# Kernel tuning notes

Measured on AMD Instinct MI355X. Metric: run time of the kernel, lower is better.

Reference implementation:

```python
import jax, jax.numpy as jnp
import numpy as np

B, DZ, M_, N_ = 2048, 256, 64, 64
GAMMA, EPS, MAXITERS = 1.0, 1e-6, 1000


def sinkhorn(Mcost):
    # entropic OT with uniform marginals r=1/m, c=1/n (ddn sinkhorn, non-logspace)
    b, h, w = Mcost.shape
    r = 1.0 / h
    c = 1.0 / w
    P = jnp.exp(-GAMMA * Mcost)
    P = P / jnp.sum(P, axis=(1, 2), keepdims=True)

    def cond_fn(state):
        P, it, err = state
        return jnp.logical_and(it < MAXITERS, err > EPS)

    def body_fn(state):
        P, it, _ = state
        alpha = jnp.sum(P, axis=2, keepdims=True)   # row sums (B,h,1)
        P = P * (r / alpha)                          # row normalize to r
        beta = jnp.sum(P, axis=1, keepdims=True)    # col sums (B,1,w)
        err = jnp.max(jnp.abs(beta - c))
        # torch loop breaks BEFORE col-normalizing when converged
        P = jnp.where(err <= EPS, P, P * (c / beta))
        return P, it + 1, err

    init_err = jnp.array(jnp.inf, dtype=Mcost.dtype)
    P, _, _ = jax.lax.while_loop(cond_fn, body_fn, (P, jnp.array(0, jnp.int32), init_err))
    return P


def setup_inputs() -> dict:
    key = jax.random.key(0)
    ks = jax.random.split(key, 7)
    H = M_ * N_
    z = jax.random.normal(ks[0], (B, DZ), dtype=jnp.float32)
    W1 = jax.random.normal(ks[1], (DZ, H), dtype=jnp.float32) * (1.0 / np.sqrt(DZ))
    b1 = jnp.zeros((H,), jnp.float32)
    W2 = jax.random.normal(ks[2], (H, H), dtype=jnp.float32) * (1.0 / np.sqrt(H))
    b2 = jnp.zeros((H,), jnp.float32)
    W3 = jax.random.normal(ks[3], (H, H), dtype=jnp.float32) * (1.0 / np.sqrt(H))
    b3 = jnp.zeros((H,), jnp.float32)
    return {"z": z, "W1": W1, "b1": b1, "W2": W2, "b2": b2, "W3": W3, "b3": b3}


def reference(z, W1, b1, W2, b2, W3, b3):
    x = jax.nn.relu(z @ W1 + b1)
    x = jax.nn.relu(x @ W2 + b2)
    x = x @ W3 + b3
    x = x.reshape(z.shape[0], M_, N_)  # (B, m, n) cost matrix
    return sinkhorn(x)
```

## Files before the change

kernel.cpp:

```cpp
#include <hip/hip_runtime.h>
#include <hip/hip_bf16.h>

typedef unsigned short ushort_t;
typedef __attribute__((ext_vector_type(8))) short bf16x8;
typedef __attribute__((ext_vector_type(4))) float f32x4;

#define MDIM 2048
#define NDIM 4096

__device__ __forceinline__ ushort_t to_bf16(float f) {
    __hip_bfloat16 h = __float2bfloat16(f);
    return *reinterpret_cast<ushort_t*>(&h);
}

__global__ void cast_bf16_kernel(const float* __restrict__ in, ushort_t* __restrict__ out, int n) {
    int i = blockIdx.x * blockDim.x + threadIdx.x;
    if (i < n) out[i] = to_bf16(in[i]);
}

__global__ void transpose_cast_kernel(const float* __restrict__ W, ushort_t* __restrict__ WT,
                                      int K, int N) {
    __shared__ float tile[32][33];
    const int tx = threadIdx.x, ty = threadIdx.y;
    const int n0 = blockIdx.x * 32, k0 = blockIdx.y * 32;
#pragma unroll
    for (int r = 0; r < 4; ++r)
        tile[ty + r * 8][tx] = W[(size_t)(k0 + ty + r * 8) * N + n0 + tx];
    __syncthreads();
    const int t = ty * 32 + tx;
    const int nl = t >> 3;
    const int kc = (t & 7) * 4;
    ushort4 o;
    o.x = to_bf16(tile[kc + 0][nl]);
    o.y = to_bf16(tile[kc + 1][nl]);
    o.z = to_bf16(tile[kc + 2][nl]);
    o.w = to_bf16(tile[kc + 3][nl]);
    *reinterpret_cast<ushort4*>(&WT[(size_t)(n0 + nl) * K + k0 + kc]) = o;
}

template <typename OutT, bool RELU>
__global__ __launch_bounds__(256, 2) void gemm_bt(const ushort_t* __restrict__ A,
                                                  const ushort_t* __restrict__ BT,
                                                  const float* __restrict__ bias,
                                                  OutT* __restrict__ C, int Kdim) {
    __shared__ __align__(16) ushort_t As[128 * 40];
    __shared__ __align__(16) ushort_t Bs[128 * 40];

    const int t = threadIdx.x;
    const int m0 = blockIdx.y * 128;
    const int n0 = blockIdx.x * 128;
    const int lane = t & 63;
    const int wid = t >> 6;
    const int quad = lane >> 4;
    const int l16 = lane & 15;
    const int wm = (wid & 1) * 64;
    const int wn = (wid >> 1) * 64;

    f32x4 acc[4][4];
#pragma unroll
    for (int i = 0; i < 4; ++i)
#pragma unroll
        for (int j = 0; j < 4; ++j) acc[i][j] = (f32x4){0.f, 0.f, 0.f, 0.f};

    const int row_a = t >> 2;
    const int cc = t & 3;

    const ushort_t* pA0 = A + (size_t)(m0 + row_a) * Kdim + cc * 8;
    const ushort_t* pA1 = A + (size_t)(m0 + row_a + 64) * Kdim + cc * 8;
    const ushort_t* pB0 = BT + (size_t)(n0 + row_a) * Kdim + cc * 8;
    const ushort_t* pB1 = BT + (size_t)(n0 + row_a + 64) * Kdim + cc * 8;

    uint4 av0 = *reinterpret_cast<const uint4*>(pA0);
    uint4 av1 = *reinterpret_cast<const uint4*>(pA1);
    uint4 bv0 = *reinterpret_cast<const uint4*>(pB0);
    uint4 bv1 = *reinterpret_cast<const uint4*>(pB1);

    for (int k0 = 0; k0 < Kdim; k0 += 32) {
        __syncthreads();
        *reinterpret_cast<uint4*>(&As[row_a * 40 + cc * 8]) = av0;
        *reinterpret_cast<uint4*>(&As[(row_a + 64) * 40 + cc * 8]) = av1;
        *reinterpret_cast<uint4*>(&Bs[row_a * 40 + cc * 8]) = bv0;
        *reinterpret_cast<uint4*>(&Bs[(row_a + 64) * 40 + cc * 8]) = bv1;
        __syncthreads();

        if (k0 + 32 < Kdim) {
            av0 = *reinterpret_cast<const uint4*>(pA0 + k0 + 32);
            av1 = *reinterpret_cast<const uint4*>(pA1 + k0 + 32);
            bv0 = *reinterpret_cast<const uint4*>(pB0 + k0 + 32);
            bv1 = *reinterpret_cast<const uint4*>(pB1 + k0 + 32);
        }

        bf16x8 af[4], bfr[4];
#pragma unroll
        for (int i = 0; i < 4; ++i)
            af[i] = *reinterpret_cast<const bf16x8*>(&As[(wm + i * 16 + l16) * 40 + quad * 8]);
#pragma unroll
        for (int j = 0; j < 4; ++j)
            bfr[j] = *reinterpret_cast<const bf16x8*>(&Bs[(wn + j * 16 + l16) * 40 + quad * 8]);
#pragma unroll
        for (int i = 0; i < 4; ++i)
#pragma unroll
            for (int j = 0; j < 4; ++j)
                acc[i][j] = __builtin_amdgcn_mfma_f32_16x16x32_bf16(af[i], bfr[j], acc[i][j], 0, 0, 0);
    }

#pragma unroll
    for (int i = 0; i < 4; ++i) {
#pragma unroll
        for (int r = 0; r < 4; ++r) {
            const int grow = m0 + wm + i * 16 + quad * 4 + r;
#pragma unroll
            for (int j = 0; j < 4; ++j) {
                const int gcol = n0 + wn + j * 16 + l16;
                float v = acc[i][j][r] + bias[gcol];
                if (RELU) v = fmaxf(v, 0.0f);
                if constexpr (sizeof(OutT) == 2) {
                    C[(size_t)grow * NDIM + gcol] = to_bf16(v);
                } else {
                    C[(size_t)grow * NDIM + gcol] = v;
                }
            }
        }
    }
}

__device__ __forceinline__ float rdl(float v, int l) {
    return __uint_as_float(__builtin_amdgcn_readlane(__float_as_uint(v), l));
}

__global__ __launch_bounds__(64) void sinkhorn_kernel(float* __restrict__ PM) {
    __shared__ __align__(16) float T[64 * 65];
    const int l = threadIdx.x;
    float* base = PM + (size_t)blockIdx.x * 4096;

    float Kcol[64];
    float Krow[64];
#pragma unroll
    for (int r = 0; r < 64; ++r)
        Kcol[r] = __expf(-base[r * 64 + l]);
#pragma unroll
    for (int r = 0; r < 64; ++r)
        T[r * 65 + l] = Kcol[r];
    __syncthreads();
#pragma unroll
    for (int c = 0; c < 64; ++c)
        Krow[c] = T[l * 65 + c];

    float a = 0.0f, b = 1.0f;
    for (int it = 0; it < 1000; ++it) {
        float t1 = 0.0f;
#pragma unroll
        for (int c = 0; c < 64; ++c)
            t1 = fmaf(Krow[c], rdl(b, c), t1);
        a = 0.015625f / t1;

        float t2 = 0.0f;
#pragma unroll
        for (int r = 0; r < 64; ++r)
            t2 = fmaf(Kcol[r], rdl(a, r), t2);
        const float err = fabsf(b * t2 - 0.015625f);
        if (__ballot(err > 1e-6f) == 0ull) break;
        b = 0.015625f / t2;
    }

#pragma unroll
    for (int r = 0; r < 64; ++r)
        base[r * 64 + l] = rdl(a, r) * Kcol[r] * b;
}

extern "C" void kernel_launch(void* const* d_in, const int* in_sizes, int n_in,
                              void* d_out, int out_size, void* d_ws, size_t ws_size,
                              hipStream_t stream) {
    const float* z  = (const float*)d_in[0];
    const float* W1 = (const float*)d_in[1];
    const float* b1 = (const float*)d_in[2];
    const float* W2 = (const float*)d_in[3];
    const float* b2 = (const float*)d_in[4];
    const float* W3 = (const float*)d_in[5];
    const float* b3 = (const float*)d_in[6];
    float* out = (float*)d_out;
    char* ws = (char*)d_ws;

    ushort_t* W2T = (ushort_t*)(ws + 0);
    ushort_t* W3T = (ushort_t*)(ws + (size_t)33554432);
    ushort_t* C1b = (ushort_t*)(ws + (size_t)67108864);
    ushort_t* C2b = (ushort_t*)(ws + (size_t)83886080);
    ushort_t* Zb  = (ushort_t*)(ws + (size_t)100663296);
    ushort_t* W1T = (ushort_t*)(ws + (size_t)101711872);

    cast_bf16_kernel<<<2048, 256, 0, stream>>>(z, Zb, MDIM * 256);
    transpose_cast_kernel<<<dim3(128, 8), dim3(32, 8), 0, stream>>>(W1, W1T, 256, 4096);
    transpose_cast_kernel<<<dim3(128, 128), dim3(32, 8), 0, stream>>>(W2, W2T, 4096, 4096);
    transpose_cast_kernel<<<dim3(128, 128), dim3(32, 8), 0, stream>>>(W3, W3T, 4096, 4096);

    gemm_bt<ushort_t, true><<<dim3(NDIM / 128, MDIM / 128), 256, 0, stream>>>(Zb, W1T, b1, C1b, 256);
    gemm_bt<ushort_t, true><<<dim3(NDIM / 128, MDIM / 128), 256, 0, stream>>>(C1b, W2T, b2, C2b, 4096);
    gemm_bt<float, false><<<dim3(NDIM / 128, MDIM / 128), 256, 0, stream>>>(C2b, W3T, b3, out, 4096);

    sinkhorn_kernel<<<2048, 64, 0, stream>>>(out);
}
```

Before: 385.3 us.

## Enlarge GEMM tile to 128x256 and double-buffer LDS with single barrier

Each GEMM block now computes a 128x256 output tile, with each wave holding a 64x128 accumulator set, and the launch grid is halved to match. Shared memory is double-buffered so the next K-slice is written to the alternate buffer after the MFMAs, leaving one barrier per iteration. The goal is more MFMA work per LDS/global load and less synchronisation. In exchange it uses more registers and LDS, drops to one block per CU, and launches only 256 blocks, which reduces latency hiding.

```diff
diff --git a/kernel.cpp b/kernel.cpp
--- a/kernel.cpp
+++ b/kernel.cpp
@@ -39,69 +39,96 @@
 }
 
 template <typename OutT, bool RELU>
-__global__ __launch_bounds__(256, 2) void gemm_bt(const ushort_t* __restrict__ A,
+__global__ __launch_bounds__(256, 1) void gemm_bt(const ushort_t* __restrict__ A,
                                                   const ushort_t* __restrict__ BT,
                                                   const float* __restrict__ bias,
                                                   OutT* __restrict__ C, int Kdim) {
-    __shared__ __align__(16) ushort_t As[128 * 40];
-    __shared__ __align__(16) ushort_t Bs[128 * 40];
+    __shared__ __align__(16) ushort_t As[2][128 * 40];
+    __shared__ __align__(16) ushort_t Bs[2][256 * 40];
 
     const int t = threadIdx.x;
     const int m0 = blockIdx.y * 128;
-    const int n0 = blockIdx.x * 128;
+    const int n0 = blockIdx.x * 256;
     const int lane = t & 63;
     const int wid = t >> 6;
     const int quad = lane >> 4;
     const int l16 = lane & 15;
     const int wm = (wid & 1) * 64;
-    const int wn = (wid >> 1) * 64;
-
-    f32x4 acc[4][4];
+    const int wn = (wid >> 1) * 128;
+
+    f32x4 acc[4][8];
 #pragma unroll
     for (int i = 0; i < 4; ++i)
 #pragma unroll
-        for (int j = 0; j < 4; ++j) acc[i][j] = (f32x4){0.f, 0.f, 0.f, 0.f};
+        for (int j = 0; j < 8; ++j) acc[i][j] = (f32x4){0.f, 0.f, 0.f, 0.f};
 
     const int row_a = t >> 2;
     const int cc = t & 3;
 
     const ushort_t* pA0 = A + (size_t)(m0 + row_a) * Kdim + cc * 8;
-    const ushort_t* pA1 = A + (size_t)(m0 + row_a + 64) * Kdim + cc * 8;
+    const ushort_t* pA1 = pA0 + (size_t)64 * Kdim;
     const ushort_t* pB0 = BT + (size_t)(n0 + row_a) * Kdim + cc * 8;
-    const ushort_t* pB1 = BT + (size_t)(n0 + row_a + 64) * Kdim + cc * 8;
-
-    uint4 av0 = *reinterpret_cast<const uint4*>(pA0);
-    uint4 av1 = *reinterpret_cast<const uint4*>(pA1);
-    uint4 bv0 = *reinterpret_cast<const uint4*>(pB0);
-    uint4 bv1 = *reinterpret_cast<const uint4*>(pB1);
-
+    const ushort_t* pB1 = pB0 + (size_t)64 * Kdim;
+    const ushort_t* pB2 = pB0 + (size_t)128 * Kdim;
+    const ushort_t* pB3 = pB0 + (size_t)192 * Kdim;
+
+    const int la0 = row_a * 40 + cc * 8;
+    const int la1 = (row_a + 64) * 40 + cc * 8;
+    const int lb0 = row_a * 40 + cc * 8;
+    const int lb1 = (row_a + 64) * 40 + cc * 8;
+    const int lb2 = (row_a + 128) * 40 + cc * 8;
+    const int lb3 = (row_a + 192) * 40 + cc * 8;
+
+    uint4 ra0 = *reinterpret_cast<const uint4*>(pA0);
+    uint4 ra1 = *reinterpret_cast<const uint4*>(pA1);
+    uint4 rb0 = *reinterpret_cast<const uint4*>(pB0);
+    uint4 rb1 = *reinterpret_cast<const uint4*>(pB1);
+    uint4 rb2 = *reinterpret_cast<const uint4*>(pB2);
+    uint4 rb3 = *reinterpret_cast<const uint4*>(pB3);
+    *reinterpret_cast<uint4*>(&As[0][la0]) = ra0;
+    *reinterpret_cast<uint4*>(&As[0][la1]) = ra1;
+    *reinterpret_cast<uint4*>(&Bs[0][lb0]) = rb0;
+    *reinterpret_cast<uint4*>(&Bs[0][lb1]) = rb1;
+    *reinterpret_cast<uint4*>(&Bs[0][lb2]) = rb2;
+    *reinterpret_cast<uint4*>(&Bs[0][lb3]) = rb3;
+    __syncthreads();
+
+    int p = 0;
     for (int k0 = 0; k0 < Kdim; k0 += 32) {
+        const bool more = (k0 + 32) < Kdim;
+        if (more) {
+            ra0 = *reinterpret_cast<const uint4*>(pA0 + k0 + 32);
+            ra1 = *reinterpret_cast<const uint4*>(pA1 + k0 + 32);
+            rb0 = *reinterpret_cast<const uint4*>(pB0 + k0 + 32);
+            rb1 = *reinterpret_cast<const uint4*>(pB1 + k0 + 32);
+            rb2 = *reinterpret_cast<const uint4*>(pB2 + k0 + 32);
+            rb3 = *reinterpret_cast<const uint4*>(pB3 + k0 + 32);
+        }
+
+        bf16x8 af[4], bfr[8];
+#pragma unroll
+        for (int i = 0; i < 4; ++i)
+            af[i] = *reinterpret_cast<const bf16x8*>(&As[p][(wm + i * 16 + l16) * 40 + quad * 8]);
+#pragma unroll
+        for (int j = 0; j < 8; ++j)
+            bfr[j] = *reinterpret_cast<const bf16x8*>(&Bs[p][(wn + j * 16 + l16) * 40 + quad * 8]);
+
+#pragma unroll
+        for (int i = 0; i < 4; ++i)
+#pragma unroll
+            for (int j = 0; j < 8; ++j)
+                acc[i][j] = __builtin_amdgcn_mfma_f32_16x16x32_bf16(af[i], bfr[j], acc[i][j], 0, 0, 0);
+
+        if (more) {
+            *reinterpret_cast<uint4*>(&As[p ^ 1][la0]) = ra0;
+            *reinterpret_cast<uint4*>(&As[p ^ 1][la1]) = ra1;
+            *reinterpret_cast<uint4*>(&Bs[p ^ 1][lb0]) = rb0;
+            *reinterpret_cast<uint4*>(&Bs[p ^ 1][lb1]) = rb1;
+            *reinterpret_cast<uint4*>(&Bs[p ^ 1][lb2]) = rb2;
+            *reinterpret_cast<uint4*>(&Bs[p ^ 1][lb3]) = rb3;
+        }
         __syncthreads();
-        *reinterpret_cast<uint4*>(&As[row_a * 40 + cc * 8]) = av0;
-        *reinterpret_cast<uint4*>(&As[(row_a + 64) * 40 + cc * 8]) = av1;
-        *reinterpret_cast<uint4*>(&Bs[row_a * 40 + cc * 8]) = bv0;
-        *reinterpret_cast<uint4*>(&Bs[(row_a + 64) * 40 + cc * 8]) = bv1;
-        __syncthreads();
-
-        if (k0 + 32 < Kdim) {
-            av0 = *reinterpret_cast<const uint4*>(pA0 + k0 + 32);
-            av1 = *reinterpret_cast<const uint4*>(pA1 + k0 + 32);
-            bv0 = *reinterpret_cast<const uint4*>(pB0 + k0 + 32);
-            bv1 = *reinterpret_cast<const uint4*>(pB1 + k0 + 32);
-        }
-
-        bf16x8 af[4], bfr[4];
-#pragma unroll
-        for (int i = 0; i < 4; ++i)
-            af[i] = *reinterpret_cast<const bf16x8*>(&As[(wm + i * 16 + l16) * 40 + quad * 8]);
-#pragma unroll
-        for (int j = 0; j < 4; ++j)
-            bfr[j] = *reinterpret_cast<const bf16x8*>(&Bs[(wn + j * 16 + l16) * 40 + quad * 8]);
-#pragma unroll
-        for (int i = 0; i < 4; ++i)
-#pragma unroll
-            for (int j = 0; j < 4; ++j)
-                acc[i][j] = __builtin_amdgcn_mfma_f32_16x16x32_bf16(af[i], bfr[j], acc[i][j], 0, 0, 0);
+        p ^= 1;
     }
 
 #pragma unroll
@@ -110,7 +137,7 @@
         for (int r = 0; r < 4; ++r) {
             const int grow = m0 + wm + i * 16 + quad * 4 + r;
 #pragma unroll
-            for (int j = 0; j < 4; ++j) {
+            for (int j = 0; j < 8; ++j) {
                 const int gcol = n0 + wn + j * 16 + l16;
                 float v = acc[i][j][r] + bias[gcol];
                 if (RELU) v = fmaxf(v, 0.0f);
@@ -193,9 +220,9 @@
     transpose_cast_kernel<<<dim3(128, 128), dim3(32, 8), 0, stream>>>(W2, W2T, 4096, 4096);
     transpose_cast_kernel<<<dim3(128, 128), dim3(32, 8), 0, stream>>>(W3, W3T, 4096, 4096);
 
-    gemm_bt<ushort_t, true><<<dim3(NDIM / 128, MDIM / 128), 256, 0, stream>>>(Zb, W1T, b1, C1b, 256);
-    gemm_bt<ushort_t, true><<<dim3(NDIM / 128, MDIM / 128), 256, 0, stream>>>(C1b, W2T, b2, C2b, 4096);
-    gemm_bt<float, false><<<dim3(NDIM / 128, MDIM / 128), 256, 0, stream>>>(C2b, W3T, b3, out, 4096);
+    gemm_bt<ushort_t, true><<<dim3(NDIM / 256, MDIM / 128), 256, 0, stream>>>(Zb, W1T, b1, C1b, 256);
+    gemm_bt<ushort_t, true><<<dim3(NDIM / 256, MDIM / 128), 256, 0, stream>>>(C1b, W2T, b2, C2b, 4096);
+    gemm_bt<float, false><<<dim3(NDIM / 256, MDIM / 128), 256, 0, stream>>>(C2b, W3T, b3, out, 4096);
 
     sinkhorn_kernel<<<2048, 64, 0, stream>>>(out);
 }
```

Result: no change. 392.1 us (+1.8%).
